# Performance work log

Hardware: AMD Instinct MI355X
Metric: run time of the kernel (lower is better)

Reference implementation:

```python
import jax, jax.numpy as jnp
import numpy as np

B, N, K, H = 8, 256, 64, 768
NUM_CLASSES = 10
D_SIM = 0.3  # self.d in the torch module


def setup_inputs() -> dict:
    key = jax.random.key(0)
    ks = jax.random.split(key, 12)
    s = 0.02  # init scale to keep 3 stacked linear GCN layers numerically tame
    return {
        "encoder_out": jax.random.normal(ks[0], (B, N, H), jnp.float32),
        "landmarks": jax.random.normal(ks[1], (K, H), jnp.float32),
        "alpha": jnp.array([0.5], jnp.float32),
        "gcn_w1": jax.random.normal(ks[2], (H, H), jnp.float32) * s,
        "gcn_b1": jnp.zeros((H,), jnp.float32),
        "gcn_w2": jax.random.normal(ks[3], (H, H), jnp.float32) * s,
        "gcn_b2": jnp.zeros((H,), jnp.float32),
        "gcn_w3": jax.random.normal(ks[4], (H, H), jnp.float32) * s,
        "gcn_b3": jnp.zeros((H,), jnp.float32),
        "fc1_w": jax.random.normal(ks[5], (1000, K * H), jnp.float32) * s,
        "fc1_b": jnp.zeros((1000,), jnp.float32),
        "fc2_w": jax.random.normal(ks[6], (100, 1000), jnp.float32) * s,
        "fc2_b": jnp.zeros((100,), jnp.float32),
        "fc3_w": jax.random.normal(ks[7], (NUM_CLASSES, 100), jnp.float32) * s,
        "fc3_b": jnp.zeros((NUM_CLASSES,), jnp.float32),
    }


def reference(encoder_out, landmarks, alpha,
              gcn_w1, gcn_b1, gcn_w2, gcn_b2, gcn_w3, gcn_b3,
              fc1_w, fc1_b, fc2_w, fc2_b, fc3_w, fc3_b):
    b, n, h = encoder_out.shape
    k = landmarks.shape[0]

    # distance_matrix: [B,N,K], min-max normalized over clusters
    diff = encoder_out[:, :, None, :] - landmarks[None, None, :, :]  # [B,N,K,H]
    dist = jnp.sqrt(jnp.sum(diff * diff, axis=-1))                   # [B,N,K]
    mn = dist.min(axis=-1, keepdims=True)
    mx = dist.max(axis=-1, keepdims=True)
    nd = (dist - mn) / (mx - mn + 1e-6)

    # probability_matrix: gaussian similarity, row-normalized
    sim = jnp.exp(-nd * nd / (2.0 * D_SIM * D_SIM))
    prob = sim / sim.sum(axis=-1, keepdims=True)  # [B,N,K]

    # compute_distance_weight: [N,N] smooth matrix
    idx = jnp.arange(n)
    dw = jnp.exp(-alpha[0] * jnp.abs(idx[:, None] - idx[None, :]).astype(jnp.float32))

    # graph_constructing: einsum('bik,bjl->bijkl') * W then sum over (k,l)
    # == bilinear form P @ W @ P^T, computed WITHOUT the 5-D tensor
    P = prob.transpose(0, 2, 1)                      # [B,K,N]
    G = jnp.einsum('bik,kl,bjl->bij', P, dw, P)      # [B,K,K]

    # cluster pooling: prob^T @ encoder_out -> [B,K,H]
    out = jnp.einsum('bnk,bnh->bkh', prob, encoder_out)
    out_ori = out  # dropout is identity at inference

    # gcn_batched: PyG GCNConv x3 on the dense graph G!=0, batched.
    # gcn_norm: add remaining self-loops, A_hat = A + I_missing,
    # out = D^-1/2 A_hat D^-1/2 (X W^T) + bias  (no nonlinearity between layers)
    A = (G != 0).astype(jnp.float32)                 # [B,K,K]
    A = jnp.maximum(A, jnp.eye(k, dtype=jnp.float32))
    deg = A.sum(axis=-1)                             # [B,K]
    dinv = jnp.where(deg > 0, 1.0 / jnp.sqrt(deg), 0.0)
    An = A * dinv[:, :, None] * dinv[:, None, :]     # normalized adjacency

    hx = out
    for w, bias in ((gcn_w1, gcn_b1), (gcn_w2, gcn_b2), (gcn_w3, gcn_b3)):
        hx = jnp.einsum('bij,bjh->bih', An, hx @ w.T) + bias
    gcn_out = hx + out  # residual inside gcn_batched

    x = (out_ori + gcn_out).reshape(b, -1)           # [B, K*H]
    x = jax.nn.gelu(x @ fc1_w.T + fc1_b, approximate=False)
    x = jax.nn.gelu(x @ fc2_w.T + fc2_b, approximate=False)
    return x @ fc3_w.T + fc3_b                       # [B, NUM_CLASSES]
```

## Files before the change

### kernel.cpp

```cpp
#include <hip/hip_runtime.h>
#include <math.h>

#define DEV __device__ __forceinline__

DEV float dot4(float4 a, float4 b){ return a.x*b.x + a.y*b.y + a.z*b.z + a.w*b.w; }

DEV float wave_sum(float v){
  #pragma unroll
  for (int off = 32; off; off >>= 1) v += __shfl_xor(v, off, 64);
  return v;
}

DEV float gelu_exact(float v){ return 0.5f * v * (1.f + erff(v * 0.70710678118654752f)); }

__global__ void k_lmT(const float* __restrict__ lm, float* __restrict__ lmT4,
                      float* __restrict__ lnorm){
  int k = blockIdx.x, t = threadIdx.x;
  __shared__ float red[256];
  float s = 0.f;
  if (t < 192){
    float4 v = *(const float4*)(lm + k*768 + 4*t);
    ((float4*)lmT4)[t*64 + k] = v;
    s = dot4(v, v);
  }
  red[t] = s; __syncthreads();
  for (int off = 128; off; off >>= 1){ if (t < off) red[t] += red[t+off]; __syncthreads(); }
  if (t == 0) lnorm[k] = red[0];
}

__global__ void k_prob(const float* __restrict__ enc, const float* __restrict__ lmT4,
                       const float* __restrict__ lnorm, float* __restrict__ prob){
  int t = threadIdx.x, lane = t & 63, wv = t >> 6;
  int row0 = blockIdx.x*8 + wv*2;
  const float4* LT = (const float4*)lmT4;
  const float4* X0 = (const float4*)(enc + (size_t)row0*768);
  const float4* X1 = (const float4*)(enc + (size_t)(row0+1)*768);
  float dot0=0.f, dot1=0.f, xn0=0.f, xn1=0.f;
  #pragma unroll 4
  for (int hg = 0; hg < 192; ++hg){
    float4 l4 = LT[hg*64 + lane];
    float4 a = X0[hg], b = X1[hg];
    dot0 += dot4(a, l4); dot1 += dot4(b, l4);
    xn0  += dot4(a, a);  xn1  += dot4(b, b);
  }
  float ln = lnorm[lane];
  float d0 = sqrtf(fmaxf(xn0 + ln - 2.f*dot0, 0.f));
  float d1 = sqrtf(fmaxf(xn1 + ln - 2.f*dot1, 0.f));
  float mn0=d0, mx0=d0, mn1=d1, mx1=d1;
  #pragma unroll
  for (int off = 32; off; off >>= 1){
    mn0 = fminf(mn0, __shfl_xor(mn0, off, 64));
    mx0 = fmaxf(mx0, __shfl_xor(mx0, off, 64));
    mn1 = fminf(mn1, __shfl_xor(mn1, off, 64));
    mx1 = fmaxf(mx1, __shfl_xor(mx1, off, 64));
  }
  float nd0 = (d0 - mn0) / (mx0 - mn0 + 1e-6f);
  float nd1 = (d1 - mn1) / (mx1 - mn1 + 1e-6f);
  float s0 = expf(nd0*nd0 * (-1.f/0.18f));
  float s1 = expf(nd1*nd1 * (-1.f/0.18f));
  float sum0 = wave_sum(s0), sum1 = wave_sum(s1);
  prob[(size_t)row0*64 + lane]     = s0 / sum0;
  prob[(size_t)(row0+1)*64 + lane] = s1 / sum1;
}

__global__ void k_pool(const float* __restrict__ enc, const float* __restrict__ prob,
                       float* __restrict__ outp, float* __restrict__ mbar){
  int b = blockIdx.x / 24, ch = blockIdx.x % 24;
  int lane = threadIdx.x & 63, wv = threadIdx.x >> 6;
  int h0 = ch*32 + wv*8;
  const float* E = enc + (size_t)b*256*768 + h0;
  const float* P = prob + (size_t)b*256*64;
  float acc[8] = {0,0,0,0,0,0,0,0};
  for (int n = 0; n < 256; ++n){
    float p = P[n*64 + lane];
    float4 e0 = *(const float4*)(E + (size_t)n*768);
    float4 e1 = *(const float4*)(E + (size_t)n*768 + 4);
    acc[0] += p*e0.x; acc[1] += p*e0.y; acc[2] += p*e0.z; acc[3] += p*e0.w;
    acc[4] += p*e1.x; acc[5] += p*e1.y; acc[6] += p*e1.z; acc[7] += p*e1.w;
  }
  float* O = outp + ((size_t)b*64 + lane)*768 + h0;
  *(float4*)O       = make_float4(acc[0],acc[1],acc[2],acc[3]);
  *(float4*)(O + 4) = make_float4(acc[4],acc[5],acc[6],acc[7]);
  #pragma unroll
  for (int j = 0; j < 8; ++j){
    float v = wave_sum(acc[j]);
    if (lane == 0) mbar[(size_t)b*768 + h0 + j] = v * (1.f/64.f);
  }
}

__global__ void k_vm768(const float* __restrict__ in, const float* __restrict__ W,
                        const float* __restrict__ bias, float* __restrict__ out){
  int lane = threadIdx.x & 63, wv = threadIdx.x >> 6;
  int j = blockIdx.x*4 + wv;
  const float4* Wr = (const float4*)(W + (size_t)j*768);
  const float4* IN = (const float4*)in;
  float acc[8] = {0,0,0,0,0,0,0,0};
  #pragma unroll
  for (int s = 0; s < 3; ++s){
    int ig = s*64 + lane;
    float4 w4 = Wr[ig];
    #pragma unroll
    for (int b = 0; b < 8; ++b) acc[b] += dot4(w4, IN[b*192 + ig]);
  }
  #pragma unroll
  for (int b = 0; b < 8; ++b){
    float v = wave_sum(acc[b]);
    if (lane == 0) out[b*768 + j] = v + bias[j];
  }
}

__global__ void k_xcat(const float* __restrict__ outp, const float* __restrict__ hx3,
                       float* __restrict__ x){
  int idx = blockIdx.x*256 + threadIdx.x;
  int h4 = idx % 192;
  int b  = idx / (192*64);
  float4 o = ((const float4*)outp)[idx];
  float4 g = ((const float4*)hx3)[b*192 + h4];
  float4 r;
  r.x = 2.f*o.x + g.x; r.y = 2.f*o.y + g.y; r.z = 2.f*o.z + g.z; r.w = 2.f*o.w + g.w;
  ((float4*)x)[idx] = r;
}

__global__ void k_fc1(const float* __restrict__ x, const float* __restrict__ W,
                      float* __restrict__ y1raw){
  int lane = threadIdx.x & 63, wv = threadIdx.x >> 6;
  int j0 = blockIdx.x*4;
  const float4* X  = (const float4*)x;
  const float4* W0 = (const float4*)(W + (size_t)(j0+0)*49152);
  const float4* W1 = (const float4*)(W + (size_t)(j0+1)*49152);
  const float4* W2 = (const float4*)(W + (size_t)(j0+2)*49152);
  const float4* W3 = (const float4*)(W + (size_t)(j0+3)*49152);
  float acc[4][8];
  #pragma unroll
  for (int jj = 0; jj < 4; ++jj)
    #pragma unroll
    for (int b = 0; b < 8; ++b) acc[jj][b] = 0.f;
  int base = wv*3072;
  for (int s = 0; s < 48; ++s){
    int ig = base + s*64 + lane;
    float4 w0 = W0[ig], w1 = W1[ig], w2 = W2[ig], w3 = W3[ig];
    #pragma unroll
    for (int b = 0; b < 8; ++b){
      float4 xv = X[b*12288 + ig];
      acc[0][b] += dot4(w0, xv); acc[1][b] += dot4(w1, xv);
      acc[2][b] += dot4(w2, xv); acc[3][b] += dot4(w3, xv);
    }
  }
  __shared__ float part[4][32];
  #pragma unroll
  for (int jj = 0; jj < 4; ++jj)
    #pragma unroll
    for (int b = 0; b < 8; ++b){
      float v = wave_sum(acc[jj][b]);
      if (lane == 0) part[wv][jj*8 + b] = v;
    }
  __syncthreads();
  if (threadIdx.x < 32){
    int jj = threadIdx.x >> 3, b = threadIdx.x & 7;
    float v = part[0][threadIdx.x] + part[1][threadIdx.x]
            + part[2][threadIdx.x] + part[3][threadIdx.x];
    y1raw[b*1000 + j0 + jj] = v;
  }
}

__global__ void k_gelu1(const float* __restrict__ y, const float* __restrict__ bias,
                        float* __restrict__ x1){
  int idx = blockIdx.x*256 + threadIdx.x;
  if (idx < 8000){
    int j = idx % 1000;
    x1[idx] = gelu_exact(y[idx] + bias[j]);
  }
}

__global__ void k_fc2(const float* __restrict__ x1, const float* __restrict__ W,
                      const float* __restrict__ bias, float* __restrict__ x2){
  int lane = threadIdx.x & 63, wv = threadIdx.x >> 6;
  int m = blockIdx.x*4 + wv;
  const float4* Wr = (const float4*)(W + (size_t)m*1000);
  const float4* X  = (const float4*)x1;
  float acc[8] = {0,0,0,0,0,0,0,0};
  for (int s = 0; s < 4; ++s){
    int jg = s*64 + lane;
    if (jg < 250){
      float4 w4 = Wr[jg];
      #pragma unroll
      for (int b = 0; b < 8; ++b) acc[b] += dot4(w4, X[b*250 + jg]);
    }
  }
  #pragma unroll
  for (int b = 0; b < 8; ++b){
    float v = wave_sum(acc[b]);
    if (lane == 0) x2[b*100 + m] = gelu_exact(v + bias[m]);
  }
}

__global__ void k_fc3(const float* __restrict__ x2, const float* __restrict__ W,
                      const float* __restrict__ bias, float* __restrict__ out){
  int t = threadIdx.x;
  if (t < 80){
    int b = t/10, c = t%10;
    float acc = bias[c];
    for (int m = 0; m < 100; ++m) acc += x2[b*100+m] * W[c*100+m];
    out[t] = acc;
  }
}

extern "C" void kernel_launch(void* const* d_in, const int* in_sizes, int n_in,
                              void* d_out, int out_size, void* d_ws, size_t ws_size,
                              hipStream_t stream){
  const float* enc = (const float*)d_in[0];
  const float* lm  = (const float*)d_in[1];
  const float* w1  = (const float*)d_in[3];
  const float* b1  = (const float*)d_in[4];
  const float* w2  = (const float*)d_in[5];
  const float* b2  = (const float*)d_in[6];
  const float* w3  = (const float*)d_in[7];
  const float* b3  = (const float*)d_in[8];
  const float* fw1 = (const float*)d_in[9];
  const float* fb1 = (const float*)d_in[10];
  const float* fw2 = (const float*)d_in[11];
  const float* fb2 = (const float*)d_in[12];
  const float* fw3 = (const float*)d_in[13];
  const float* fb3 = (const float*)d_in[14];

  float* ws    = (float*)d_ws;
  float* lmT4  = ws;
  float* lnorm = lmT4  + 49152;
  float* prob  = lnorm + 64;
  float* outp  = prob  + 131072;
  float* mbar  = outp  + 393216;
  float* hx1   = mbar  + 6144;
  float* hx2   = hx1   + 6144;
  float* hx3   = hx2   + 6144;
  float* xcat  = hx3   + 6144;
  float* y1raw = xcat  + 393216;
  float* x1    = y1raw + 8000;
  float* x2    = x1    + 8000;
  float* out   = (float*)d_out;

  k_lmT  <<<64, 256, 0, stream>>>(lm, lmT4, lnorm);
  k_prob <<<256,256, 0, stream>>>(enc, lmT4, lnorm, prob);
  k_pool <<<192,256, 0, stream>>>(enc, prob, outp, mbar);
  k_vm768<<<192,256, 0, stream>>>(mbar, w1, b1, hx1);
  k_vm768<<<192,256, 0, stream>>>(hx1,  w2, b2, hx2);
  k_vm768<<<192,256, 0, stream>>>(hx2,  w3, b3, hx3);
  k_xcat <<<384,256, 0, stream>>>(outp, hx3, xcat);
  k_fc1  <<<250,256, 0, stream>>>(xcat, fw1, y1raw);
  k_gelu1<<<32, 256, 0, stream>>>(y1raw, fb1, x1);
  k_fc2  <<<25, 256, 0, stream>>>(x1, fw2, fb2, x2);
  k_fc3  <<<1, 128, 0, stream>>>(x2, fw3, fb3, out);
}
```

Measured before the change: 142.7 us.

## Split fc1 reduction across blocks and widen pool grid for more parallelism

The fc1 GEMV is split along the reduction dimension into 8 chunks, giving 2000 blocks instead of 250. The partial sums go to a workspace buffer and are reduced in the GELU kernel. The pooling kernel now processes 4 columns per wave across 384 blocks instead of 8 columns across 192, and the prob loop unroll rises to 8. The aim is to fill the GPU's CUs during the bandwidth-bound fc1 weight stream (about 197MB), at the cost of extra partial writes and a second-pass reduction.

Result: slower. 413.6 us (+189.9%).

```diff
diff --git a/kernel.cpp b/kernel.cpp
--- a/kernel.cpp
+++ b/kernel.cpp
@@ -36,7 +36,7 @@
   const float4* X0 = (const float4*)(enc + (size_t)row0*768);
   const float4* X1 = (const float4*)(enc + (size_t)(row0+1)*768);
   float dot0=0.f, dot1=0.f, xn0=0.f, xn1=0.f;
-  #pragma unroll 4
+  #pragma unroll 8
   for (int hg = 0; hg < 192; ++hg){
     float4 l4 = LT[hg*64 + lane];
     float4 a = X0[hg], b = X1[hg];
@@ -65,24 +65,22 @@
 
 __global__ void k_pool(const float* __restrict__ enc, const float* __restrict__ prob,
                        float* __restrict__ outp, float* __restrict__ mbar){
-  int b = blockIdx.x / 24, ch = blockIdx.x % 24;
-  int lane = threadIdx.x & 63, wv = threadIdx.x >> 6;
-  int h0 = ch*32 + wv*8;
+  int b = blockIdx.x / 48, ch = blockIdx.x % 48;
+  int lane = threadIdx.x & 63, wv = threadIdx.x >> 6;
+  int h0 = ch*16 + wv*4;
   const float* E = enc + (size_t)b*256*768 + h0;
   const float* P = prob + (size_t)b*256*64;
-  float acc[8] = {0,0,0,0,0,0,0,0};
+  float acc[4] = {0,0,0,0};
+  #pragma unroll 4
   for (int n = 0; n < 256; ++n){
     float p = P[n*64 + lane];
     float4 e0 = *(const float4*)(E + (size_t)n*768);
-    float4 e1 = *(const float4*)(E + (size_t)n*768 + 4);
     acc[0] += p*e0.x; acc[1] += p*e0.y; acc[2] += p*e0.z; acc[3] += p*e0.w;
-    acc[4] += p*e1.x; acc[5] += p*e1.y; acc[6] += p*e1.z; acc[7] += p*e1.w;
   }
   float* O = outp + ((size_t)b*64 + lane)*768 + h0;
-  *(float4*)O       = make_float4(acc[0],acc[1],acc[2],acc[3]);
-  *(float4*)(O + 4) = make_float4(acc[4],acc[5],acc[6],acc[7]);
-  #pragma unroll
-  for (int j = 0; j < 8; ++j){
+  *(float4*)O = make_float4(acc[0],acc[1],acc[2],acc[3]);
+  #pragma unroll
+  for (int j = 0; j < 4; ++j){
     float v = wave_sum(acc[j]);
     if (lane == 0) mbar[(size_t)b*768 + h0 + j] = v * (1.f/64.f);
   }
@@ -121,10 +119,11 @@
   ((float4*)x)[idx] = r;
 }
 
-__global__ void k_fc1(const float* __restrict__ x, const float* __restrict__ W,
-                      float* __restrict__ y1raw){
-  int lane = threadIdx.x & 63, wv = threadIdx.x >> 6;
-  int j0 = blockIdx.x*4;
+__global__ void k_fc1p(const float* __restrict__ x, const float* __restrict__ W,
+                       float* __restrict__ part_out){
+  int lane = threadIdx.x & 63, wv = threadIdx.x >> 6;
+  int jg = blockIdx.x >> 3, kc = blockIdx.x & 7;
+  int j0 = jg*4;
   const float4* X  = (const float4*)x;
   const float4* W0 = (const float4*)(W + (size_t)(j0+0)*49152);
   const float4* W1 = (const float4*)(W + (size_t)(j0+1)*49152);
@@ -135,8 +134,9 @@
   for (int jj = 0; jj < 4; ++jj)
     #pragma unroll
     for (int b = 0; b < 8; ++b) acc[jj][b] = 0.f;
-  int base = wv*3072;
-  for (int s = 0; s < 48; ++s){
+  int base = kc*1536 + wv*384;
+  #pragma unroll
+  for (int s = 0; s < 6; ++s){
     int ig = base + s*64 + lane;
     float4 w0 = W0[ig], w1 = W1[ig], w2 = W2[ig], w3 = W3[ig];
     #pragma unroll
@@ -156,19 +156,23 @@
     }
   __syncthreads();
   if (threadIdx.x < 32){
-    int jj = threadIdx.x >> 3, b = threadIdx.x & 7;
     float v = part[0][threadIdx.x] + part[1][threadIdx.x]
             + part[2][threadIdx.x] + part[3][threadIdx.x];
-    y1raw[b*1000 + j0 + jj] = v;
-  }
-}
-
-__global__ void k_gelu1(const float* __restrict__ y, const float* __restrict__ bias,
-                        float* __restrict__ x1){
+    part_out[blockIdx.x*32 + threadIdx.x] = v;
+  }
+}
+
+__global__ void k_fc1red(const float* __restrict__ part, const float* __restrict__ bias,
+                         float* __restrict__ x1){
   int idx = blockIdx.x*256 + threadIdx.x;
   if (idx < 8000){
-    int j = idx % 1000;
-    x1[idx] = gelu_exact(y[idx] + bias[j]);
+    int j = idx % 1000, b = idx / 1000;
+    int jg = j >> 2, jj = j & 3;
+    float v = 0.f;
+    #pragma unroll
+    for (int kc = 0; kc < 8; ++kc)
+      v += part[(jg*8 + kc)*32 + jj*8 + b];
+    x1[idx] = gelu_exact(v + bias[j]);
   }
 }
 
@@ -233,20 +237,20 @@
   float* hx2   = hx1   + 6144;
   float* hx3   = hx2   + 6144;
   float* xcat  = hx3   + 6144;
-  float* y1raw = xcat  + 393216;
-  float* x1    = y1raw + 8000;
+  float* fc1p  = xcat  + 393216;
+  float* x1    = fc1p  + 64000;
   float* x2    = x1    + 8000;
   float* out   = (float*)d_out;
 
-  k_lmT  <<<64, 256, 0, stream>>>(lm, lmT4, lnorm);
-  k_prob <<<256,256, 0, stream>>>(enc, lmT4, lnorm, prob);
-  k_pool <<<192,256, 0, stream>>>(enc, prob, outp, mbar);
-  k_vm768<<<192,256, 0, stream>>>(mbar, w1, b1, hx1);
-  k_vm768<<<192,256, 0, stream>>>(hx1,  w2, b2, hx2);
-  k_vm768<<<192,256, 0, stream>>>(hx2,  w3, b3, hx3);
-  k_xcat <<<384,256, 0, stream>>>(outp, hx3, xcat);
-  k_fc1  <<<250,256, 0, stream>>>(xcat, fw1, y1raw);
-  k_gelu1<<<32, 256, 0, stream>>>(y1raw, fb1, x1);
-  k_fc2  <<<25, 256, 0, stream>>>(x1, fw2, fb2, x2);
-  k_fc3  <<<1, 128, 0, stream>>>(x2, fw3, fb3, out);
-}
+  k_lmT   <<<64,  256, 0, stream>>>(lm, lmT4, lnorm);
+  k_prob  <<<256, 256, 0, stream>>>(enc, lmT4, lnorm, prob);
+  k_pool  <<<384, 256, 0, stream>>>(enc, prob, outp, mbar);
+  k_vm768 <<<192, 256, 0, stream>>>(mbar, w1, b1, hx1);
+  k_vm768 <<<192, 256, 0, stream>>>(hx1,  w2, b2, hx2);
+  k_vm768 <<<192, 256, 0, stream>>>(hx2,  w3, b3, hx3);
+  k_xcat  <<<384, 256, 0, stream>>>(outp, hx3, xcat);
+  k_fc1p  <<<2000,256, 0, stream>>>(xcat, fw1, fc1p);
+  k_fc1red<<<32,  256, 0, stream>>>(fc1p, fb1, x1);
+  k_fc2   <<<25,  256, 0, stream>>>(x1, fw2, fb2, x2);
+  k_fc3   <<<1,   128, 0, stream>>>(x2, fw3, fb3, out);
+}
```
